# Performance work log

Measured on AMD Instinct MI355X. Metric: run time of the kernel, lower is better.

Reference implementation:

```python
import jax, jax.numpy as jnp
from jax import lax
import numpy as np

B, C0, C1 = 4, 128, 256
HF = WF = 256
HC = WC = 128
N_CROPS = 2048
WS0, WS1 = 8, 10
PAD0, PAD1 = 0, 1
STRIDE = 8
NW = (WF + 2 * PAD0 - WS0) // STRIDE + 1  # 32 windows per row (same for both crops)


def setup_inputs() -> dict:
    key = jax.random.key(0)
    ks = jax.random.split(key, 16)
    inp = {
        'x0_fine': jax.random.normal(ks[0], (B, C0, HF, WF), jnp.float32),
        'x0_coarse': jax.random.normal(ks[1], (B, C1, HC, WC), jnp.float32),
        'x1_fine': jax.random.normal(ks[2], (B, C0, HF, WF), jnp.float32),
        'x1_coarse': jax.random.normal(ks[3], (B, C1, HC, WC), jnp.float32),
        'proj0_w': jax.random.normal(ks[4], (C1, C0, 1, 1), jnp.float32) * 0.05,
        'proj_last_w': jax.random.normal(ks[5], (C1, C1, 1, 1), jnp.float32) * 0.05,
        'fuse_w1': jax.random.normal(ks[6], (C1, C1, 3, 3), jnp.float32) * 0.02,
        'bn_gamma': jnp.ones((C1,), jnp.float32),
        'bn_beta': jnp.zeros((C1,), jnp.float32),
        'bn_mean': jax.random.normal(ks[7], (C1,), jnp.float32) * 0.1,
        'bn_var': jax.random.uniform(ks[8], (C1,), jnp.float32) + 0.5,
        'fuse_w2': jax.random.normal(ks[9], (C0, C1, 3, 3), jnp.float32) * 0.02,
        'b_idx': jax.random.randint(ks[10], (N_CROPS,), 0, B, jnp.int32),
        'i_idx': jax.random.randint(ks[11], (N_CROPS,), 0, NW * NW, jnp.int32),
        'j_idx': jax.random.randint(ks[12], (N_CROPS,), 0, NW * NW, jnp.int32),
    }
    return inp


def conv2d(x, w, pad):
    return lax.conv_general_dilated(x, w, (1, 1), [(pad, pad), (pad, pad)],
                                    dimension_numbers=('NCHW', 'OIHW', 'NCHW'))


def up2_align_corners(x):
    # bilinear upsample x2 with align_corners=True, separable along H then W
    def interp(x, axis):
        n_in = x.shape[axis]
        n_out = 2 * n_in
        pos = jnp.arange(n_out, dtype=x.dtype) * ((n_in - 1) / (n_out - 1))
        i0 = jnp.clip(jnp.floor(pos).astype(jnp.int32), 0, n_in - 2)
        w = pos - i0.astype(x.dtype)
        a = jnp.take(x, i0, axis=axis)
        b = jnp.take(x, i0 + 1, axis=axis)
        shp = [1] * x.ndim
        shp[axis] = n_out
        w = w.reshape(shp)
        return a * (1 - w) + b * w
    return interp(interp(x, 2), 3)


def fuse(fine, coarse, proj0_w, proj_last_w, fuse_w1, bn_gamma, bn_beta, bn_mean, bn_var, fuse_w2):
    x0 = conv2d(coarse, proj_last_w, 0)                 # projs[-1]
    x0 = conv2d(fine, proj0_w, 0) + up2_align_corners(x0)
    y = conv2d(x0, fuse_w1, 1)
    inv = lax.rsqrt(bn_var + 1e-5)
    y = (y - bn_mean[None, :, None, None]) * (bn_gamma * inv)[None, :, None, None] + bn_beta[None, :, None, None]
    y = jnp.where(y >= 0, y, 0.01 * y)                  # LeakyReLU
    return conv2d(y, fuse_w2, 1)


def crop_windows(x, ws, pad, b, idx):
    # direct sparse window gather; avoids materializing the dense unfold tensor
    xp = jnp.pad(x, ((0, 0), (0, 0), (pad, pad), (pad, pad)))
    nW = (x.shape[3] + 2 * pad - ws) // STRIDE + 1
    r0 = (idx // nW) * STRIDE
    c0 = (idx % nW) * STRIDE
    rows = r0[:, None] + jnp.arange(ws)                 # [n, ws]
    cols = c0[:, None] + jnp.arange(ws)                 # [n, ws]
    crops = xp[b[:, None, None], :, rows[:, :, None], cols[:, None, :]]  # [n, ws, ws, C]
    return jnp.transpose(crops, (0, 3, 1, 2))           # [n, C, ws, ws]


def reference(x0_fine, x0_coarse, x1_fine, x1_coarse, proj0_w, proj_last_w,
              fuse_w1, bn_gamma, bn_beta, bn_mean, bn_var, fuse_w2,
              b_idx, i_idx, j_idx):
    # shapes equal -> concat, fuse once, chunk (matches torch branch)
    fine = jnp.concatenate([x0_fine, x1_fine], 0)
    coarse = jnp.concatenate([x0_coarse, x1_coarse], 0)
    y = fuse(fine, coarse, proj0_w, proj_last_w, fuse_w1, bn_gamma, bn_beta, bn_mean, bn_var, fuse_w2)
    x0, x1 = y[:B], y[B:]
    x0_cropped = crop_windows(x0, WS0, PAD0, b_idx, i_idx)
    x1_cropped = crop_windows(x1, WS1, PAD1, b_idx, j_idx)
    return (x0_cropped, x1_cropped)
```

## Files before the change

kernel.cpp:

```cpp
#include <hip/hip_runtime.h>

typedef __attribute__((ext_vector_type(8))) __bf16 bf16x8;
typedef __attribute__((ext_vector_type(4))) float f32x4;
typedef __attribute__((ext_vector_type(16))) float f32x16;

__device__ __forceinline__ unsigned short fbf(float f) {
  union { float f; unsigned u; } x; x.f = f;
  unsigned r = x.u + 0x7fffu + ((x.u >> 16) & 1u);
  return (unsigned short)(r >> 16);
}
__device__ __forceinline__ float bf2f(unsigned short h) {
  union { unsigned u; float f; } x; x.u = ((unsigned)h) << 16;
  return x.f;
}

#define OFF_WPL 0u
#define OFF_WP0 131072u
#define OFF_WT1 196608u
#define OFF_WT2 1376256u
#define OFF_BNS 1966080u
#define OFF_BNB 1967104u
#define OFF_T1  4194304u
#define OFF_X0  (OFF_T1 + 67108864u)
#define OFF_Y   (OFF_X0 + 268435456u)
#define OFF_YF  OFF_T1

__global__ void prep_kernel(const float* __restrict__ pl, const float* __restrict__ p0,
                            const float* __restrict__ w1, const float* __restrict__ w2,
                            const float* __restrict__ gam, const float* __restrict__ bet,
                            const float* __restrict__ mean, const float* __restrict__ var,
                            unsigned short* __restrict__ wpl, unsigned short* __restrict__ wp0,
                            unsigned short* __restrict__ wt1, unsigned short* __restrict__ wt2,
                            float* __restrict__ bns, float* __restrict__ bnb) {
  int t = blockIdx.x * blockDim.x + threadIdx.x;
  int stride = gridDim.x * blockDim.x;
  for (int i = t; i < 65536; i += stride) wpl[i] = fbf(pl[i]);
  for (int i = t; i < 32768; i += stride) wp0[i] = fbf(p0[i]);
  for (int i = t; i < 589824; i += stride) {
    int e = i & 7, l = (i >> 3) & 63, ks = (i >> 9) & 1;
    int cib = (i >> 10) & 7, cb = (i >> 13) & 7, tap = i >> 16;
    int ci = cib * 32 + ks * 16 + (l >> 5) * 8 + e;
    int co = cb * 32 + (l & 31);
    wt1[i] = fbf(w1[(co * 256 + ci) * 9 + tap]);
  }
  for (int i = t; i < 294912; i += stride) {
    int e = i & 7, l = (i >> 3) & 63, ks = (i >> 9) & 1;
    int cib = (i >> 10) & 7, cb = (i >> 13) & 3, tap = i >> 15;
    int ci = cib * 32 + ks * 16 + (l >> 5) * 8 + e;
    int co = cb * 32 + (l & 31);
    wt2[i] = fbf(w2[(co * 256 + ci) * 9 + tap]);
  }
  for (int i = t; i < 256; i += stride) {
    float s = gam[i] * rsqrtf(var[i] + 1e-5f);
    bns[i] = s; bnb[i] = bet[i] - mean[i] * s;
  }
}

template <int K, int HW, int WD, int EPI>
__global__ __launch_bounds__(512) void gemm1x1_kernel(
    const float* __restrict__ srcA, const float* __restrict__ srcB,
    const unsigned short* __restrict__ wmat,
    unsigned short* __restrict__ outp,
    const unsigned short* __restrict__ t1) {
  __shared__ unsigned short in_lds[128 * 32];
  __shared__ unsigned short w_lds[128 * 32];
  const int tid = threadIdx.x;
  const int pix0 = blockIdx.x * 128;
  const int co0 = blockIdx.y * 128;
  const int n = pix0 / HW;
  const int rem = pix0 % HW;
  const int h = rem / WD;
  const int w0 = rem % WD;
  const float* src = (n < 4) ? (srcA + (size_t)n * K * HW) : (srcB + (size_t)(n - 4) * K * HW);
  const float* rowbase = src + (size_t)h * WD + w0;
  const int wv = tid >> 6, lane = tid & 63;
  const int pw = wv >> 1, cw = wv & 1;
  const int l15 = lane & 15, k8 = lane >> 4;
  f32x4 zero = {0.f, 0.f, 0.f, 0.f};
  f32x4 acc[2][4];
#pragma unroll
  for (int i = 0; i < 2; i++)
#pragma unroll
    for (int j = 0; j < 4; j++) acc[i][j] = zero;
  const int sci = tid >> 4;
  const int sps = (tid & 15) * 8;
  const int wrow = tid >> 2, wsg = tid & 3;
  for (int cib = 0; cib < K / 32; ++cib) {
    int ci0 = cib * 32;
    __syncthreads();
    {
      const float* p = rowbase + (size_t)(ci0 + sci) * HW + sps;
      float4 v0 = *(const float4*)p;
      float4 v1 = *(const float4*)(p + 4);
      float vv[8] = {v0.x, v0.y, v0.z, v0.w, v1.x, v1.y, v1.z, v1.w};
#pragma unroll
      for (int i = 0; i < 8; i++) {
        int row = sps + i;
        int g = (sci >> 3) ^ ((row >> 1) & 3);
        in_lds[row * 32 + g * 8 + (sci & 7)] = fbf(vv[i]);
      }
    }
    {
      int4 v = *(const int4*)&wmat[(size_t)(co0 + wrow) * K + ci0 + wsg * 8];
      *(int4*)&w_lds[wrow * 32 + ((wsg ^ ((wrow >> 1) & 3)) << 3)] = v;
    }
    __syncthreads();
    bf16x8 b[4];
#pragma unroll
    for (int nf = 0; nf < 4; nf++) {
      int row = cw * 64 + nf * 16 + l15;
      b[nf] = *(const bf16x8*)&w_lds[row * 32 + ((k8 ^ ((row >> 1) & 3)) << 3)];
    }
#pragma unroll
    for (int mf = 0; mf < 2; mf++) {
      int row = pw * 32 + mf * 16 + l15;
      bf16x8 a = *(const bf16x8*)&in_lds[row * 32 + ((k8 ^ ((row >> 1) & 3)) << 3)];
#pragma unroll
      for (int nf = 0; nf < 4; nf++)
        acc[mf][nf] = __builtin_amdgcn_mfma_f32_16x16x32_bf16(a, b[nf], acc[mf][nf], 0, 0, 0);
    }
  }
  float fh = 0.f; int i0 = 0;
  if (EPI == 1) {
    float ph = (float)h * (127.0f / 255.0f);
    i0 = (int)ph; if (i0 > 126) i0 = 126;
    fh = ph - (float)i0;
  }
#pragma unroll
  for (int mf = 0; mf < 2; mf++) {
#pragma unroll
    for (int nf = 0; nf < 4; nf++) {
      int co = co0 + cw * 64 + nf * 16 + l15;
#pragma unroll
      for (int r = 0; r < 4; r++) {
        int m = pw * 32 + mf * 16 + k8 * 4 + r;
        float v = acc[mf][nf][r];
        if (EPI == 1) {
          int ww = w0 + m;
          float pww = (float)ww * (127.0f / 255.0f);
          int j0 = (int)pww; if (j0 > 126) j0 = 126;
          float fw = pww - (float)j0;
          const unsigned short* tb = t1 + ((size_t)(n * 128 + i0) * 128 + j0) * 256 + co;
          float a00 = bf2f(tb[0]);
          float a01 = bf2f(tb[256]);
          float a10 = bf2f(tb[128 * 256]);
          float a11 = bf2f(tb[128 * 256 + 256]);
          float top = a00 + fw * (a01 - a00);
          float bot = a10 + fw * (a11 - a10);
          v += top + fh * (bot - top);
        }
        outp[(size_t)(pix0 + m) * 256 + co] = fbf(v);
      }
    }
  }
}

template <int COT, int BNRELU>
__global__ __launch_bounds__(256, 2) void conv3x3_kernel(
    const unsigned short* __restrict__ inp,
    const unsigned short* __restrict__ wtr,
    unsigned short* __restrict__ outp,
    const float* __restrict__ bns, const float* __restrict__ bnb) {
  constexpr int WPT = COT / 32;
  __shared__ unsigned short xl[2][4 * 204 * 8];
  const int tid = threadIdx.x;
  const int bx = blockIdx.x;
  const int n = bx >> 9;
  const int h0 = ((bx >> 3) & 63) * 4;
  const int w0 = (bx & 7) * 32;
  const int co0 = blockIdx.y * 128;
  const int lane = tid & 63, cw = tid >> 6;
  const int l31 = lane & 31, lh = lane >> 5;
  const int cb = (co0 >> 5) + cw;

  f32x16 acc[4];
#pragma unroll
  for (int m = 0; m < 4; m++)
#pragma unroll
    for (int r = 0; r < 16; r++) acc[m][r] = 0.f;

#define FRAG_ADDR(tap, ks, cc) ((((size_t)((tap) * WPT + cb) * 8 + (cc)) * 2 + (ks)) * 512 + lane * 8)

  bf16x8 B[3][3][2];
#pragma unroll
  for (int kh = 0; kh < 3; kh++)
#pragma unroll
    for (int kw = 0; kw < 3; kw++)
#pragma unroll
      for (int ks = 0; ks < 2; ks++)
        B[kh][kw][ks] = *(const bf16x8*)&wtr[FRAG_ADDR(kh * 3 + kw, ks, 0)];

  const size_t nbase = (size_t)n * 256 * 256 * 256;
  for (int s = tid; s < 816; s += 256) {
    int p = s >> 2, g = s & 3;
    int row = p / 34, col = p - row * 34;
    int gh = h0 + row - 1, gw = w0 + col - 1;
    int4 v = make_int4(0, 0, 0, 0);
    if ((unsigned)gh < 256u && (unsigned)gw < 256u)
      v = *(const int4*)&inp[nbase + ((size_t)gh * 256 + gw) * 256 + g * 8];
    *(int4*)&xl[0][(g * 204 + p) * 8] = v;
  }
  __syncthreads();

  for (int cib = 0; cib < 8; ++cib) {
    const int cin = (cib + 1) & 7;
    int4 vr[4]; bool va[4]; int ldst[4];
    if (cib < 7) {
#pragma unroll
      for (int q = 0; q < 4; ++q) {
        int s = tid + q * 256;
        va[q] = s < 816;
        int p = s >> 2, g = s & 3;
        int row = p / 34, col = p - row * 34;
        int gh = h0 + row - 1, gw = w0 + col - 1;
        ldst[q] = (g * 204 + p) * 8;
        vr[q] = make_int4(0, 0, 0, 0);
        if (va[q] && (unsigned)gh < 256u && (unsigned)gw < 256u)
          vr[q] = *(const int4*)&inp[nbase + ((size_t)gh * 256 + gw) * 256 + cin * 32 + g * 8];
      }
    }
    const unsigned short* xb = xl[cib & 1];
    bf16x8 af[2][6];
#pragma unroll
    for (int kw = 0; kw < 3; kw++)
#pragma unroll
      for (int ks = 0; ks < 2; ks++)
        af[0][kw * 2 + ks] = *(const bf16x8*)&xb[((ks * 2 + lh) * 204 + l31 + kw) * 8];
    __builtin_amdgcn_s_setprio(1);
#pragma unroll
    for (int r = 0; r < 6; ++r) {
      const int cur = r & 1, nxt = cur ^ 1;
      if (r < 5) {
#pragma unroll
        for (int kw = 0; kw < 3; kw++)
#pragma unroll
          for (int ks = 0; ks < 2; ks++)
            af[nxt][kw * 2 + ks] =
                *(const bf16x8*)&xb[((ks * 2 + lh) * 204 + (r + 1) * 34 + l31 + kw) * 8];
      }
#pragma unroll
      for (int kw = 0; kw < 3; kw++)
#pragma unroll
        for (int ks = 0; ks < 2; ks++)
#pragma unroll
          for (int kh = 0; kh < 3; kh++) {
            int m = r - kh;
            if (m >= 0 && m < 4)
              acc[m] = __builtin_amdgcn_mfma_f32_32x32x16_bf16(af[cur][kw * 2 + ks],
                                                               B[kh][kw][ks], acc[m], 0, 0, 0);
          }
      if (r >= 3) {
        int kh = r - 3;
#pragma unroll
        for (int kw = 0; kw < 3; ++kw)
#pragma unroll
          for (int ks = 0; ks < 2; ++ks)
            B[kh][kw][ks] = *(const bf16x8*)&wtr[FRAG_ADDR(kh * 3 + kw, ks, cin)];
      }
    }
    __builtin_amdgcn_s_setprio(0);
    if (cib < 7) {
#pragma unroll
      for (int q = 0; q < 4; ++q)
        if (va[q]) *(int4*)&xl[cin & 1][ldst[q]] = vr[q];
      __syncthreads();
    }
  }
#undef FRAG_ADDR

  const int coL = co0 + cw * 32 + l31;
  float s = 1.f, t = 0.f;
  if (BNRELU) { s = bns[coL]; t = bnb[coL]; }
#pragma unroll
  for (int m = 0; m < 4; ++m) {
    int h = h0 + m;
    size_t rowb = (((size_t)(n * 256 + h) * 256) + w0) * COT + coL;
#pragma unroll
    for (int r = 0; r < 16; ++r) {
      int wofs = (r & 3) + 8 * (r >> 2) + 4 * lh;
      float v = acc[m][r];
      if (BNRELU) { v = v * s + t; v = (v >= 0.f) ? v : 0.01f * v; }
      outp[rowb + (size_t)wofs * COT] = fbf(v);
    }
  }
}

template <int WS, int PAD>
__global__ __launch_bounds__(256) void gather_kernel(
    const unsigned short* __restrict__ yf,
    const int* __restrict__ bidx, const int* __restrict__ widx,
    int bofs, float* __restrict__ outp) {
  const int WS2 = WS * WS;
  __shared__ unsigned short tile[WS * WS * 136];
  const int crop = blockIdx.x, tid = threadIdx.x;
  const int b = bidx[crop] + bofs;
  const int idx = widx[crop];
  const int r0 = (idx >> 5) * 8, c0 = (idx & 31) * 8;
  for (int t = tid; t < WS2 * 16; t += 256) {
    int p = t >> 4, sg = t & 15;
    int r = p / WS, cc = p - r * WS;
    int sr = r0 + r - PAD, sc = c0 + cc - PAD;
    int4 v = make_int4(0, 0, 0, 0);
    if ((unsigned)sr < 256u && (unsigned)sc < 256u)
      v = *(const int4*)&yf[(((size_t)(b * 256 + sr) * 256) + sc) * 128 + sg * 8];
    *(int4*)&tile[p * 136 + sg * 8] = v;
  }
  __syncthreads();
  float* dst = outp + (size_t)crop * 128 * WS2;
  for (int o = tid; o < 128 * WS2; o += 256) {
    int c = o / WS2, p = o - c * WS2;
    dst[o] = bf2f(tile[p * 136 + c]);
  }
}

extern "C" void kernel_launch(void* const* d_in, const int* in_sizes, int n_in,
                              void* d_out, int out_size, void* d_ws, size_t ws_size,
                              hipStream_t stream) {
  const float* x0f = (const float*)d_in[0];
  const float* x0c = (const float*)d_in[1];
  const float* x1f = (const float*)d_in[2];
  const float* x1c = (const float*)d_in[3];
  const float* p0w = (const float*)d_in[4];
  const float* plw = (const float*)d_in[5];
  const float* fw1 = (const float*)d_in[6];
  const float* gam = (const float*)d_in[7];
  const float* bet = (const float*)d_in[8];
  const float* men = (const float*)d_in[9];
  const float* var = (const float*)d_in[10];
  const float* fw2 = (const float*)d_in[11];
  const int* b_idx = (const int*)d_in[12];
  const int* i_idx = (const int*)d_in[13];
  const int* j_idx = (const int*)d_in[14];
  (void)in_sizes; (void)n_in; (void)out_size; (void)ws_size;

  char* ws = (char*)d_ws;
  unsigned short* wpl = (unsigned short*)(ws + OFF_WPL);
  unsigned short* wp0 = (unsigned short*)(ws + OFF_WP0);
  unsigned short* wt1 = (unsigned short*)(ws + OFF_WT1);
  unsigned short* wt2 = (unsigned short*)(ws + OFF_WT2);
  float* bns = (float*)(ws + OFF_BNS);
  float* bnb = (float*)(ws + OFF_BNB);
  unsigned short* t1 = (unsigned short*)(ws + OFF_T1);
  unsigned short* x0 = (unsigned short*)(ws + OFF_X0);
  unsigned short* y = (unsigned short*)(ws + OFF_Y);
  unsigned short* yf = (unsigned short*)(ws + OFF_YF);
  float* out0 = (float*)d_out;
  float* out1 = out0 + (size_t)2048 * 128 * 64;

  prep_kernel<<<512, 256, 0, stream>>>(plw, p0w, fw1, fw2, gam, bet, men, var,
                                       wpl, wp0, wt1, wt2, bns, bnb);
  gemm1x1_kernel<256, 16384, 128, 0><<<dim3(1024, 2), 512, 0, stream>>>(x0c, x1c, wpl, t1, nullptr);
  gemm1x1_kernel<128, 65536, 256, 1><<<dim3(4096, 2), 512, 0, stream>>>(x0f, x1f, wp0, x0, t1);
  conv3x3_kernel<256, 1><<<dim3(4096, 2), 256, 0, stream>>>(x0, wt1, y, bns, bnb);
  conv3x3_kernel<128, 0><<<dim3(4096, 1), 256, 0, stream>>>(y, wt2, yf, nullptr, nullptr);
  gather_kernel<8, 0><<<2048, 256, 0, stream>>>(yf, b_idx, i_idx, 0, out0);
  gather_kernel<10, 1><<<2048, 256, 0, stream>>>(yf, b_idx, j_idx, 4, out1);
}
```

Measured before the change: 1.216 ms.

## Compute all output channels per block in 1x1 GEMMs and 3x3 convs

The 1x1 GEMM kernels now compute all 256 output channels per block instead of splitting channels across two grid.y blocks, so each input tile is loaded and converted to bf16 once instead of twice. The 3x3 convs move to 512-thread blocks that cover every output channel, and the second conv also covers two row groups per block, which removes duplicated halo and input loads. The cost is more accumulator registers per thread (the 1x1 accumulators double), larger LDS tiles and a new launch bound of 4, which may lower occupancy or cause spills.

New measurement: 4.098 ms. 237% more time.

```diff
diff --git a/kernel.cpp b/kernel.cpp
--- a/kernel.cpp
+++ b/kernel.cpp
@@ -63,10 +63,9 @@
     unsigned short* __restrict__ outp,
     const unsigned short* __restrict__ t1) {
   __shared__ unsigned short in_lds[128 * 32];
-  __shared__ unsigned short w_lds[128 * 32];
+  __shared__ unsigned short w_lds[256 * 32];
   const int tid = threadIdx.x;
   const int pix0 = blockIdx.x * 128;
-  const int co0 = blockIdx.y * 128;
   const int n = pix0 / HW;
   const int rem = pix0 % HW;
   const int h = rem / WD;
@@ -77,14 +76,15 @@
   const int pw = wv >> 1, cw = wv & 1;
   const int l15 = lane & 15, k8 = lane >> 4;
   f32x4 zero = {0.f, 0.f, 0.f, 0.f};
-  f32x4 acc[2][4];
-#pragma unroll
-  for (int i = 0; i < 2; i++)
-#pragma unroll
-    for (int j = 0; j < 4; j++) acc[i][j] = zero;
+  f32x4 acc[2][2][4];
+#pragma unroll
+  for (int c = 0; c < 2; c++)
+#pragma unroll
+    for (int i = 0; i < 2; i++)
+#pragma unroll
+      for (int j = 0; j < 4; j++) acc[c][i][j] = zero;
   const int sci = tid >> 4;
   const int sps = (tid & 15) * 8;
-  const int wrow = tid >> 2, wsg = tid & 3;
   for (int cib = 0; cib < K / 32; ++cib) {
     int ci0 = cib * 32;
     __syncthreads();
@@ -100,24 +100,31 @@
         in_lds[row * 32 + g * 8 + (sci & 7)] = fbf(vv[i]);
       }
     }
-    {
-      int4 v = *(const int4*)&wmat[(size_t)(co0 + wrow) * K + ci0 + wsg * 8];
-      *(int4*)&w_lds[wrow * 32 + ((wsg ^ ((wrow >> 1) & 3)) << 3)] = v;
+#pragma unroll
+    for (int q = 0; q < 2; q++) {
+      int s = tid + q * 512;
+      int row = s >> 2, sg = s & 3;
+      int4 v = *(const int4*)&wmat[(size_t)row * K + ci0 + sg * 8];
+      *(int4*)&w_lds[row * 32 + ((sg ^ ((row >> 1) & 3)) << 3)] = v;
     }
     __syncthreads();
-    bf16x8 b[4];
-#pragma unroll
-    for (int nf = 0; nf < 4; nf++) {
-      int row = cw * 64 + nf * 16 + l15;
-      b[nf] = *(const bf16x8*)&w_lds[row * 32 + ((k8 ^ ((row >> 1) & 3)) << 3)];
-    }
+    bf16x8 b[2][4];
+#pragma unroll
+    for (int ch = 0; ch < 2; ch++)
+#pragma unroll
+      for (int nf = 0; nf < 4; nf++) {
+        int row = ch * 128 + cw * 64 + nf * 16 + l15;
+        b[ch][nf] = *(const bf16x8*)&w_lds[row * 32 + ((k8 ^ ((row >> 1) & 3)) << 3)];
+      }
 #pragma unroll
     for (int mf = 0; mf < 2; mf++) {
       int row = pw * 32 + mf * 16 + l15;
       bf16x8 a = *(const bf16x8*)&in_lds[row * 32 + ((k8 ^ ((row >> 1) & 3)) << 3)];
 #pragma unroll
-      for (int nf = 0; nf < 4; nf++)
-        acc[mf][nf] = __builtin_amdgcn_mfma_f32_16x16x32_bf16(a, b[nf], acc[mf][nf], 0, 0, 0);
+      for (int ch = 0; ch < 2; ch++)
+#pragma unroll
+        for (int nf = 0; nf < 4; nf++)
+          acc[ch][mf][nf] = __builtin_amdgcn_mfma_f32_16x16x32_bf16(a, b[ch][nf], acc[ch][mf][nf], 0, 0, 0);
     }
   }
   float fh = 0.f; int i0 = 0;
@@ -127,51 +134,59 @@
     fh = ph - (float)i0;
   }
 #pragma unroll
-  for (int mf = 0; mf < 2; mf++) {
-#pragma unroll
-    for (int nf = 0; nf < 4; nf++) {
-      int co = co0 + cw * 64 + nf * 16 + l15;
-#pragma unroll
-      for (int r = 0; r < 4; r++) {
-        int m = pw * 32 + mf * 16 + k8 * 4 + r;
-        float v = acc[mf][nf][r];
-        if (EPI == 1) {
-          int ww = w0 + m;
-          float pww = (float)ww * (127.0f / 255.0f);
-          int j0 = (int)pww; if (j0 > 126) j0 = 126;
-          float fw = pww - (float)j0;
-          const unsigned short* tb = t1 + ((size_t)(n * 128 + i0) * 128 + j0) * 256 + co;
-          float a00 = bf2f(tb[0]);
-          float a01 = bf2f(tb[256]);
-          float a10 = bf2f(tb[128 * 256]);
-          float a11 = bf2f(tb[128 * 256 + 256]);
-          float top = a00 + fw * (a01 - a00);
-          float bot = a10 + fw * (a11 - a10);
-          v += top + fh * (bot - top);
+  for (int ch = 0; ch < 2; ch++) {
+#pragma unroll
+    for (int mf = 0; mf < 2; mf++) {
+#pragma unroll
+      for (int nf = 0; nf < 4; nf++) {
+        int co = ch * 128 + cw * 64 + nf * 16 + l15;
+#pragma unroll
+        for (int r = 0; r < 4; r++) {
+          int m = pw * 32 + mf * 16 + k8 * 4 + r;
+          float v = acc[ch][mf][nf][r];
+          if (EPI == 1) {
+            int ww = w0 + m;
+            float pww = (float)ww * (127.0f / 255.0f);
+            int j0 = (int)pww; if (j0 > 126) j0 = 126;
+            float fw = pww - (float)j0;
+            const unsigned short* tb = t1 + ((size_t)(n * 128 + i0) * 128 + j0) * 256 + co;
+            float a00 = bf2f(tb[0]);
+            float a01 = bf2f(tb[256]);
+            float a10 = bf2f(tb[128 * 256]);
+            float a11 = bf2f(tb[128 * 256 + 256]);
+            float top = a00 + fw * (a01 - a00);
+            float bot = a10 + fw * (a11 - a10);
+            v += top + fh * (bot - top);
+          }
+          outp[(size_t)(pix0 + m) * 256 + co] = fbf(v);
         }
-        outp[(size_t)(pix0 + m) * 256 + co] = fbf(v);
-      }
-    }
-  }
-}
-
-template <int COT, int BNRELU>
-__global__ __launch_bounds__(256, 2) void conv3x3_kernel(
+      }
+    }
+  }
+}
+
+template <int COT, int BNRELU, int HG>
+__global__ __launch_bounds__(512, 4) void conv3x3_kernel(
     const unsigned short* __restrict__ inp,
     const unsigned short* __restrict__ wtr,
     unsigned short* __restrict__ outp,
     const float* __restrict__ bns, const float* __restrict__ bnb) {
   constexpr int WPT = COT / 32;
-  __shared__ unsigned short xl[2][4 * 204 * 8];
+  constexpr int ROWS = HG * 4 + 2;
+  constexpr int PIXR = ROWS * 34;
+  constexpr int NI4 = PIXR * 4;
+  constexpr int NQ = (NI4 + 511) / 512;
+  constexpr int HB = 256 / (HG * 4);
+  __shared__ unsigned short xl[2][4 * PIXR * 8];
   const int tid = threadIdx.x;
   const int bx = blockIdx.x;
-  const int n = bx >> 9;
-  const int h0 = ((bx >> 3) & 63) * 4;
-  const int w0 = (bx & 7) * 32;
-  const int co0 = blockIdx.y * 128;
-  const int lane = tid & 63, cw = tid >> 6;
+  const int n = bx / (HB * 8);
+  const int rem = bx % (HB * 8);
+  const int h0 = (rem >> 3) * (HG * 4);
+  const int w0 = (rem & 7) * 32;
+  const int lane = tid & 63, wv = tid >> 6;
+  const int cg = wv % WPT, hg = wv / WPT;
   const int l31 = lane & 31, lh = lane >> 5;
-  const int cb = (co0 >> 5) + cw;
 
   f32x16 acc[4];
 #pragma unroll
@@ -179,7 +194,7 @@
 #pragma unroll
     for (int r = 0; r < 16; r++) acc[m][r] = 0.f;
 
-#define FRAG_ADDR(tap, ks, cc) ((((size_t)((tap) * WPT + cb) * 8 + (cc)) * 2 + (ks)) * 512 + lane * 8)
+#define FRAG_ADDR(tap, ks, cc) ((((size_t)((tap) * WPT + cg) * 8 + (cc)) * 2 + (ks)) * 512 + lane * 8)
 
   bf16x8 B[3][3][2];
 #pragma unroll
@@ -191,29 +206,29 @@
         B[kh][kw][ks] = *(const bf16x8*)&wtr[FRAG_ADDR(kh * 3 + kw, ks, 0)];
 
   const size_t nbase = (size_t)n * 256 * 256 * 256;
-  for (int s = tid; s < 816; s += 256) {
+  for (int s = tid; s < NI4; s += 512) {
     int p = s >> 2, g = s & 3;
     int row = p / 34, col = p - row * 34;
     int gh = h0 + row - 1, gw = w0 + col - 1;
     int4 v = make_int4(0, 0, 0, 0);
     if ((unsigned)gh < 256u && (unsigned)gw < 256u)
       v = *(const int4*)&inp[nbase + ((size_t)gh * 256 + gw) * 256 + g * 8];
-    *(int4*)&xl[0][(g * 204 + p) * 8] = v;
+    *(int4*)&xl[0][(g * PIXR + p) * 8] = v;
   }
   __syncthreads();
 
   for (int cib = 0; cib < 8; ++cib) {
     const int cin = (cib + 1) & 7;
-    int4 vr[4]; bool va[4]; int ldst[4];
+    int4 vr[NQ]; bool va[NQ]; int ldst[NQ];
     if (cib < 7) {
 #pragma unroll
-      for (int q = 0; q < 4; ++q) {
-        int s = tid + q * 256;
-        va[q] = s < 816;
+      for (int q = 0; q < NQ; ++q) {
+        int s = tid + q * 512;
+        va[q] = s < NI4;
         int p = s >> 2, g = s & 3;
         int row = p / 34, col = p - row * 34;
         int gh = h0 + row - 1, gw = w0 + col - 1;
-        ldst[q] = (g * 204 + p) * 8;
+        ldst[q] = (g * PIXR + p) * 8;
         vr[q] = make_int4(0, 0, 0, 0);
         if (va[q] && (unsigned)gh < 256u && (unsigned)gw < 256u)
           vr[q] = *(const int4*)&inp[nbase + ((size_t)gh * 256 + gw) * 256 + cin * 32 + g * 8];
@@ -225,7 +240,8 @@
     for (int kw = 0; kw < 3; kw++)
 #pragma unroll
       for (int ks = 0; ks < 2; ks++)
-        af[0][kw * 2 + ks] = *(const bf16x8*)&xb[((ks * 2 + lh) * 204 + l31 + kw) * 8];
+        af[0][kw * 2 + ks] =
+            *(const bf16x8*)&xb[((ks * 2 + lh) * PIXR + hg * 4 * 34 + l31 + kw) * 8];
     __builtin_amdgcn_s_setprio(1);
 #pragma unroll
     for (int r = 0; r < 6; ++r) {
@@ -236,7 +252,7 @@
 #pragma unroll
           for (int ks = 0; ks < 2; ks++)
             af[nxt][kw * 2 + ks] =
-                *(const bf16x8*)&xb[((ks * 2 + lh) * 204 + (r + 1) * 34 + l31 + kw) * 8];
+                *(const bf16x8*)&xb[((ks * 2 + lh) * PIXR + (hg * 4 + r + 1) * 34 + l31 + kw) * 8];
       }
 #pragma unroll
       for (int kw = 0; kw < 3; kw++)
@@ -261,19 +277,19 @@
     __builtin_amdgcn_s_setprio(0);
     if (cib < 7) {
 #pragma unroll
-      for (int q = 0; q < 4; ++q)
+      for (int q = 0; q < NQ; ++q)
         if (va[q]) *(int4*)&xl[cin & 1][ldst[q]] = vr[q];
       __syncthreads();
     }
   }
 #undef FRAG_ADDR
 
-  const int coL = co0 + cw * 32 + l31;
+  const int coL = cg * 32 + l31;
   float s = 1.f, t = 0.f;
   if (BNRELU) { s = bns[coL]; t = bnb[coL]; }
 #pragma unroll
   for (int m = 0; m < 4; ++m) {
-    int h = h0 + m;
+    int h = h0 + hg * 4 + m;
     size_t rowb = (((size_t)(n * 256 + h) * 256) + w0) * COT + coL;
 #pragma unroll
     for (int r = 0; r < 16; ++r) {
@@ -349,10 +365,10 @@
 
   prep_kernel<<<512, 256, 0, stream>>>(plw, p0w, fw1, fw2, gam, bet, men, var,
                                        wpl, wp0, wt1, wt2, bns, bnb);
-  gemm1x1_kernel<256, 16384, 128, 0><<<dim3(1024, 2), 512, 0, stream>>>(x0c, x1c, wpl, t1, nullptr);
-  gemm1x1_kernel<128, 65536, 256, 1><<<dim3(4096, 2), 512, 0, stream>>>(x0f, x1f, wp0, x0, t1);
-  conv3x3_kernel<256, 1><<<dim3(4096, 2), 256, 0, stream>>>(x0, wt1, y, bns, bnb);
-  conv3x3_kernel<128, 0><<<dim3(4096, 1), 256, 0, stream>>>(y, wt2, yf, nullptr, nullptr);
+  gemm1x1_kernel<256, 16384, 128, 0><<<dim3(1024), 512, 0, stream>>>(x0c, x1c, wpl, t1, nullptr);
+  gemm1x1_kernel<128, 65536, 256, 1><<<dim3(4096), 512, 0, stream>>>(x0f, x1f, wp0, x0, t1);
+  conv3x3_kernel<256, 1, 1><<<dim3(4096), 512, 0, stream>>>(x0, wt1, y, bns, bnb);
+  conv3x3_kernel<128, 0, 2><<<dim3(2048), 512, 0, stream>>>(y, wt2, yf, nullptr, nullptr);
   gather_kernel<8, 0><<<2048, 256, 0, stream>>>(yf, b_idx, i_idx, 0, out0);
   gather_kernel<10, 1><<<2048, 256, 0, stream>>>(yf, b_idx, j_idx, 4, out1);
 }
```

## Stage conv3x3 input via direct global-to-LDS loads with triple buffering and XCD-aware block swizzle

Applied to the files above, without the earlier changes.

Rewrites the conv3x3 input staging so each channel block is loaded straight into LDS with global_load_lds, bypassing registers. Three LDS buffers are used with a two-stage prefetch, and each iteration waits with a partial vmcnt before its barrier. Out-of-bounds halo pixels now read from a zeroed scratch buffer. The grid is flattened and swizzled so that blocks sharing spatial tiles and output-channel halves sit close in dispatch order across XCDs. The launch-bounds occupancy hint is dropped. Risks: the hand-tuned vmcnt counts must match the number of loads actually issued, and the larger LDS footprint may lower occupancy.

After: 1.221 ms. No clear change (+0.4%).

```diff
diff --git a/kernel.cpp b/kernel.cpp
--- a/kernel.cpp
+++ b/kernel.cpp
@@ -20,6 +20,7 @@
 #define OFF_WT2 1376256u
 #define OFF_BNS 1966080u
 #define OFF_BNB 1967104u
+#define OFF_ZG  1968128u
 #define OFF_T1  4194304u
 #define OFF_X0  (OFF_T1 + 67108864u)
 #define OFF_Y   (OFF_X0 + 268435456u)
@@ -31,7 +32,8 @@
                             const float* __restrict__ mean, const float* __restrict__ var,
                             unsigned short* __restrict__ wpl, unsigned short* __restrict__ wp0,
                             unsigned short* __restrict__ wt1, unsigned short* __restrict__ wt2,
-                            float* __restrict__ bns, float* __restrict__ bnb) {
+                            float* __restrict__ bns, float* __restrict__ bnb,
+                            int* __restrict__ zg) {
   int t = blockIdx.x * blockDim.x + threadIdx.x;
   int stride = gridDim.x * blockDim.x;
   for (int i = t; i < 65536; i += stride) wpl[i] = fbf(pl[i]);
@@ -50,6 +52,7 @@
     int co = cb * 32 + (l & 31);
     wt2[i] = fbf(w2[(co * 256 + ci) * 9 + tap]);
   }
+  for (int i = t; i < 1024; i += stride) zg[i] = 0;
   for (int i = t; i < 256; i += stride) {
     float s = gam[i] * rsqrtf(var[i] + 1e-5f);
     bns[i] = s; bnb[i] = bet[i] - mean[i] * s;
@@ -155,20 +158,24 @@
   }
 }
 
-template <int COT, int BNRELU>
-__global__ __launch_bounds__(256, 2) void conv3x3_kernel(
+template <int COT, int BNRELU, int NCO>
+__global__ __launch_bounds__(256) void conv3x3_kernel(
     const unsigned short* __restrict__ inp,
     const unsigned short* __restrict__ wtr,
     unsigned short* __restrict__ outp,
-    const float* __restrict__ bns, const float* __restrict__ bnb) {
+    const float* __restrict__ bns, const float* __restrict__ bnb,
+    const unsigned short* __restrict__ zg) {
   constexpr int WPT = COT / 32;
-  __shared__ unsigned short xl[2][4 * 204 * 8];
+  constexpr int NB8 = 4096 * NCO / 8;
+  __shared__ unsigned short xl[3][6528];
   const int tid = threadIdx.x;
-  const int bx = blockIdx.x;
-  const int n = bx >> 9;
-  const int h0 = ((bx >> 3) & 63) * 4;
-  const int w0 = (bx & 7) * 32;
-  const int co0 = blockIdx.y * 128;
+  int bx = blockIdx.x;
+  int sx = (bx & 7) * NB8 + (bx >> 3);
+  int co0, sp;
+  if (NCO == 2) { co0 = (sx & 1) * 128; sp = sx >> 1; } else { co0 = 0; sp = sx; }
+  const int n = sp >> 9;
+  const int h0 = ((sp >> 3) & 63) * 4;
+  const int w0 = (sp & 7) * 32;
   const int lane = tid & 63, cw = tid >> 6;
   const int l31 = lane & 31, lh = lane >> 5;
   const int cb = (co0 >> 5) + cw;
@@ -191,35 +198,36 @@
         B[kh][kw][ks] = *(const bf16x8*)&wtr[FRAG_ADDR(kh * 3 + kw, ks, 0)];
 
   const size_t nbase = (size_t)n * 256 * 256 * 256;
-  for (int s = tid; s < 816; s += 256) {
-    int p = s >> 2, g = s & 3;
+  const unsigned short* srcq[4];
+#pragma unroll
+  for (int q = 0; q < 4; ++q) {
+    int p = q * 64 + lane;
     int row = p / 34, col = p - row * 34;
     int gh = h0 + row - 1, gw = w0 + col - 1;
-    int4 v = make_int4(0, 0, 0, 0);
-    if ((unsigned)gh < 256u && (unsigned)gw < 256u)
-      v = *(const int4*)&inp[nbase + ((size_t)gh * 256 + gw) * 256 + g * 8];
-    *(int4*)&xl[0][(g * 204 + p) * 8] = v;
-  }
-  __syncthreads();
+    bool v = ((unsigned)gh < 256u) && ((unsigned)gw < 256u) && (p < 204);
+    srcq[q] = v ? (inp + nbase + (((size_t)gh * 256 + gw) * 256 + cw * 8)) : zg;
+  }
+
+  auto stage = [&](int buf) {
+#pragma unroll
+    for (int q = 0; q < 4; ++q) {
+      if (q < 3 || lane < 12) {
+        __builtin_amdgcn_global_load_lds(
+            (const __attribute__((address_space(1))) unsigned int*)srcq[q],
+            (__attribute__((address_space(3))) unsigned int*)(&xl[buf][(cw * 204 + q * 64) * 8]),
+            16, 0, 0);
+      }
+      srcq[q] += 32;
+    }
+  };
+
+  stage(0);
+  asm volatile("s_waitcnt vmcnt(0)\ns_barrier" ::: "memory");
 
   for (int cib = 0; cib < 8; ++cib) {
-    const int cin = (cib + 1) & 7;
-    int4 vr[4]; bool va[4]; int ldst[4];
-    if (cib < 7) {
-#pragma unroll
-      for (int q = 0; q < 4; ++q) {
-        int s = tid + q * 256;
-        va[q] = s < 816;
-        int p = s >> 2, g = s & 3;
-        int row = p / 34, col = p - row * 34;
-        int gh = h0 + row - 1, gw = w0 + col - 1;
-        ldst[q] = (g * 204 + p) * 8;
-        vr[q] = make_int4(0, 0, 0, 0);
-        if (va[q] && (unsigned)gh < 256u && (unsigned)gw < 256u)
-          vr[q] = *(const int4*)&inp[nbase + ((size_t)gh * 256 + gw) * 256 + cin * 32 + g * 8];
-      }
-    }
-    const unsigned short* xb = xl[cib & 1];
+    if (cib == 0) { stage(1); stage(2); }
+    else if (cib < 6) stage((cib + 2) % 3);
+    const unsigned short* xb = xl[cib % 3];
     bf16x8 af[2][6];
 #pragma unroll
     for (int kw = 0; kw < 3; kw++)
@@ -249,22 +257,18 @@
               acc[m] = __builtin_amdgcn_mfma_f32_32x32x16_bf16(af[cur][kw * 2 + ks],
                                                                B[kh][kw][ks], acc[m], 0, 0, 0);
           }
-      if (r >= 3) {
+      if (r >= 3 && cib < 7) {
         int kh = r - 3;
 #pragma unroll
         for (int kw = 0; kw < 3; ++kw)
 #pragma unroll
           for (int ks = 0; ks < 2; ++ks)
-            B[kh][kw][ks] = *(const bf16x8*)&wtr[FRAG_ADDR(kh * 3 + kw, ks, cin)];
+            B[kh][kw][ks] = *(const bf16x8*)&wtr[FRAG_ADDR(kh * 3 + kw, ks, cib + 1)];
       }
     }
     __builtin_amdgcn_s_setprio(0);
-    if (cib < 7) {
-#pragma unroll
-      for (int q = 0; q < 4; ++q)
-        if (va[q]) *(int4*)&xl[cin & 1][ldst[q]] = vr[q];
-      __syncthreads();
-    }
+    if (cib < 6)      asm volatile("s_waitcnt vmcnt(13)\ns_barrier" ::: "memory");
+    else if (cib < 7) asm volatile("s_waitcnt vmcnt(9)\ns_barrier" ::: "memory");
   }
 #undef FRAG_ADDR
 
@@ -340,6 +344,7 @@
   unsigned short* wt2 = (unsigned short*)(ws + OFF_WT2);
   float* bns = (float*)(ws + OFF_BNS);
   float* bnb = (float*)(ws + OFF_BNB);
+  unsigned short* zg = (unsigned short*)(ws + OFF_ZG);
   unsigned short* t1 = (unsigned short*)(ws + OFF_T1);
   unsigned short* x0 = (unsigned short*)(ws + OFF_X0);
   unsigned short* y = (unsigned short*)(ws + OFF_Y);
@@ -348,11 +353,11 @@
   float* out1 = out0 + (size_t)2048 * 128 * 64;
 
   prep_kernel<<<512, 256, 0, stream>>>(plw, p0w, fw1, fw2, gam, bet, men, var,
-                                       wpl, wp0, wt1, wt2, bns, bnb);
+                                       wpl, wp0, wt1, wt2, bns, bnb, (int*)zg);
   gemm1x1_kernel<256, 16384, 128, 0><<<dim3(1024, 2), 512, 0, stream>>>(x0c, x1c, wpl, t1, nullptr);
   gemm1x1_kernel<128, 65536, 256, 1><<<dim3(4096, 2), 512, 0, stream>>>(x0f, x1f, wp0, x0, t1);
-  conv3x3_kernel<256, 1><<<dim3(4096, 2), 256, 0, stream>>>(x0, wt1, y, bns, bnb);
-  conv3x3_kernel<128, 0><<<dim3(4096, 1), 256, 0, stream>>>(y, wt2, yf, nullptr, nullptr);
+  conv3x3_kernel<256, 1, 2><<<dim3(8192), 256, 0, stream>>>(x0, wt1, y, bns, bnb, zg);
+  conv3x3_kernel<128, 0, 1><<<dim3(4096), 256, 0, stream>>>(y, wt2, yf, nullptr, nullptr, zg);
   gather_kernel<8, 0><<<2048, 256, 0, stream>>>(yf, b_idx, i_idx, 0, out0);
   gather_kernel<10, 1><<<2048, 256, 0, stream>>>(yf, b_idx, j_idx, 4, out1);
 }
```
